# Performance work log

Hardware: AMD Instinct MI355X
Metric: run time of the kernel (lower is better)

The kernel has to match this reference:

```python
import jax, jax.numpy as jnp
import numpy as np

# WGS84 constants
_A = 6378137.0
_E2 = 6.69437999014e-3  # first eccentricity squared

ALPHA = 1.0
GAMMA = 2.0
DYNAMIC_GAMMA = True
SCALE_FACTOR = 1.0


def _geodetic_to_ecef(lat_rad, lon_rad, h):
    sl, cl = jnp.sin(lat_rad), jnp.cos(lat_rad)
    so, co = jnp.sin(lon_rad), jnp.cos(lon_rad)
    N = _A / jnp.sqrt(1.0 - _E2 * sl * sl)
    x = (N + h) * cl * co
    y = (N + h) * cl * so
    z = (N * (1.0 - _E2) + h) * sl
    return jnp.stack([x, y, z], axis=-1)


def setup_inputs() -> dict:
    key = jax.random.key(0)
    k1, k2, k3, k4 = jax.random.split(key, 4)
    B = 4_000_000
    lat = jax.random.uniform(k1, (B,), jnp.float32, -80.0, 80.0)    # degrees
    lon = jax.random.uniform(k2, (B,), jnp.float32, -180.0, 180.0)  # degrees
    h = jax.random.uniform(k3, (B,), jnp.float32, 0.0, 1000.0)      # meters
    targets = jnp.stack([lat, lon, h], axis=1)
    ref_ecef = _geodetic_to_ecef(jnp.deg2rad(lat), jnp.deg2rad(lon), h)
    # predicted ECEF = true ECEF + ~meters of noise -> realistic GNSS error
    inputs = ref_ecef + 2.0 * jax.random.normal(k4, (B, 3), jnp.float32)
    return {"inputs": inputs, "targets": targets}


def _ecef_to_enu(pred_ecef, gt_geodetic):
    # Batched version of the per-sample ecef_to_enu_torch loop.
    lat = jnp.deg2rad(gt_geodetic[:, 0])
    lon = jnp.deg2rad(gt_geodetic[:, 1])
    h = gt_geodetic[:, 2]
    ref = _geodetic_to_ecef(lat, lon, h)
    d = pred_ecef - ref  # [B,3]
    sl, cl = jnp.sin(lat), jnp.cos(lat)
    so, co = jnp.sin(lon), jnp.cos(lon)
    dx, dy, dz = d[:, 0], d[:, 1], d[:, 2]
    e = -so * dx + co * dy
    n = -sl * co * dx - sl * so * dy + cl * dz
    u = cl * co * dx + cl * so * dy + sl * dz
    return jnp.stack([e, n, u], axis=1)  # [B,3]


def reference(inputs, targets):
    enu_errors = _ecef_to_enu(inputs, targets)                 # [B,3]
    squared_dist = jnp.sqrt(jnp.sum(enu_errors * enu_errors, axis=1))  # L2 norm [B]
    base_loss = squared_dist
    if DYNAMIC_GAMMA:
        dyn_gamma = GAMMA * jnp.exp(-SCALE_FACTOR * base_loss)
    else:
        dyn_gamma = GAMMA
    focal_weight = jnp.power(1.0 - jnp.sqrt(squared_dist / (jnp.max(squared_dist) + 1e-8)), dyn_gamma)
    focal_loss = ALPHA * focal_weight * base_loss
    return jnp.sqrt(jnp.mean(focal_loss * focal_loss))
```

## Files before the change

### kernel.cpp

```cpp
#include <hip/hip_runtime.h>
#include <hip/hip_fp16.h>
#include <math.h>


#define THREADS 256
#define PART_CAP 8192
#define BMAX_OFF 64
#define PART_OFF (64 + PART_CAP * 4)
#define DIST_OFF (1 << 20)

__device__ __forceinline__ void sincos8(const double* __restrict__ x,
                                        double* __restrict__ s,
                                        double* __restrict__ c) {
    const double TWO_OVER_PI = 0.636619772367581343076;
    const double PIO2_HI = 1.57079632679489655800e+00;
    const double PIO2_LO = 6.12323399573676603587e-17;

    double kd[8], r[8], r2[8];
    int q[8];
#pragma unroll
    for (int j = 0; j < 8; ++j) {
        kd[j] = rint(x[j] * TWO_OVER_PI);
        q[j] = ((int)kd[j]) & 3;
    }
#pragma unroll
    for (int j = 0; j < 8; ++j) {
        double rr = fma(-kd[j], PIO2_HI, x[j]);
        r[j] = fma(-kd[j], PIO2_LO, rr);
        r2[j] = r[j] * r[j];
    }
    double ps[8], pc[8];
#pragma unroll
    for (int j = 0; j < 8; ++j) { ps[j] = -2.50507602534068634195e-08;
                                  pc[j] =  2.08757232129817482790e-09; }
#pragma unroll
    for (int j = 0; j < 8; ++j) { ps[j] = fma(ps[j], r2[j],  2.75573137070700676789e-06);
                                  pc[j] = fma(pc[j], r2[j], -2.75573143513906633035e-07); }
#pragma unroll
    for (int j = 0; j < 8; ++j) { ps[j] = fma(ps[j], r2[j], -1.98412698298579493134e-04);
                                  pc[j] = fma(pc[j], r2[j],  2.48015872894767294178e-05); }
#pragma unroll
    for (int j = 0; j < 8; ++j) { ps[j] = fma(ps[j], r2[j],  8.33333333332248946124e-03);
                                  pc[j] = fma(pc[j], r2[j], -1.38888888888741095749e-03); }
#pragma unroll
    for (int j = 0; j < 8; ++j) { ps[j] = fma(ps[j], r2[j], -1.66666666666666324348e-01);
                                  pc[j] = fma(pc[j], r2[j],  4.16666666666666019037e-02); }
#pragma unroll
    for (int j = 0; j < 8; ++j) {
        double sv = fma(r2[j] * r[j], ps[j], r[j]);
        double cv = fma(r2[j] * r2[j], pc[j], fma(-0.5, r2[j], 1.0));
        double sr = (q[j] & 1) ? cv : sv;
        double cr = (q[j] & 1) ? sv : cv;
        s[j] = (q[j] & 2) ? -sr : sr;
        c[j] = ((q[j] + 1) & 2) ? -cr : cr;
    }
}

__device__ __forceinline__ void dist_group4(const float* __restrict__ lat,
                                            const float* __restrict__ lon,
                                            const float* __restrict__ hh,
                                            const float* __restrict__ px,
                                            const float* __restrict__ py,
                                            const float* __restrict__ pz,
                                            float* __restrict__ dout) {
    const float D2R = (float)0.017453292519943295;
    double x[8], s8[8], c8[8];
#pragma unroll
    for (int j = 0; j < 4; ++j) x[j] = (double)(lat[j] * D2R);
#pragma unroll
    for (int j = 0; j < 4; ++j) x[4 + j] = (double)(lon[j] * D2R);
    sincos8(x, s8, c8);

    const double A = 6378137.0, E2 = 0.00669437999014;
#pragma unroll
    for (int j = 0; j < 4; ++j) {
        double sl = s8[j], cl = c8[j], so = s8[4 + j], co = c8[4 + j];
        double h = (double)hh[j];
        double w = fma(-E2 * sl, sl, 1.0);
        double y = fma(-0.5, w, 1.5);
        y = y * fma(-0.5 * w, y * y, 1.5);
        y = y * fma(-0.5 * w, y * y, 1.5);
        double N = A * y, Nh = N + h;
        double X = Nh * cl * co;
        double Y = Nh * cl * so;
        double Z = fma(N, -E2, N + h) * sl;
        double dx = (double)px[j] - X;
        double dy = (double)py[j] - Y;
        double dz = (double)pz[j] - Z;
        dout[j] = sqrtf((float)(dx * dx + dy * dy + dz * dz));
    }
}

__device__ __forceinline__ float dist_one(float latd, float lond, float hf,
                                          float pxx, float pyy, float pzz) {
    float lat[4] = {latd, latd, latd, latd}, lon[4] = {lond, lond, lond, lond};
    float hh[4] = {hf, hf, hf, hf};
    float px[4] = {pxx, pxx, pxx, pxx}, py[4] = {pyy, pyy, pyy, pyy}, pz[4] = {pzz, pzz, pzz, pzz};
    float d[4];
    dist_group4(lat, lon, hh, px, py, pz, d);
    return d[0];
}

#define UNPACK4(ta, tb, tc, lat, lon, hh)                         \
    float lat[4] = {ta.x, ta.w, tb.z, tc.y};                      \
    float lon[4] = {ta.y, tb.x, tb.w, tc.z};                      \
    float hh[4]  = {ta.z, tb.y, tc.x, tc.w};

__device__ __forceinline__ void store_half4(__half* p, float d0, float d1, float d2, float d3) {
    union { __half2 h2[2]; uint2 u; } pk;
    pk.h2[0] = __floats2half2_rn(d0, d1);
    pk.h2[1] = __floats2half2_rn(d2, d3);
    *(uint2*)p = pk.u;
}

__global__ __launch_bounds__(THREADS, 3)
void k_pass1(const float* __restrict__ inp, const float* __restrict__ tgt,
             __half* __restrict__ dist_arr, float* __restrict__ blockmax, long B) {
    long ngroups = (B + 3) >> 2;
    long nthreads = (long)gridDim.x * blockDim.x;
    long gstride = 2 * nthreads;
    float lmax = 0.0f;
    for (long g = (long)blockIdx.x * blockDim.x + threadIdx.x; g < ngroups; g += gstride) {
        long gA = g;
        long gB = g + nthreads;
        long baseA = gA << 2;
        long baseB = gB << 2;
        bool fastA = (baseA + 3 < B);
        bool fastB = (gB < ngroups) && (baseB + 3 < B);

        if (fastA && fastB) {
            const float4* tA = (const float4*)(tgt + 3 * baseA);
            const float4* pA = (const float4*)(inp + 3 * baseA);
            const float4* tB = (const float4*)(tgt + 3 * baseB);
            const float4* pB = (const float4*)(inp + 3 * baseB);
            float4 ta0 = tA[0], ta1 = tA[1], ta2 = tA[2];
            float4 pa0 = pA[0], pa1 = pA[1], pa2 = pA[2];
            float4 tb0 = tB[0], tb1 = tB[1], tb2 = tB[2];
            float4 pb0 = pB[0], pb1 = pB[1], pb2 = pB[2];

            UNPACK4(ta0, ta1, ta2, latA, lonA, hhA);
            UNPACK4(pa0, pa1, pa2, pxA, pyA, pzA);
            float dA[4];
            dist_group4(latA, lonA, hhA, pxA, pyA, pzA, dA);

            UNPACK4(tb0, tb1, tb2, latB, lonB, hhB);
            UNPACK4(pb0, pb1, pb2, pxB, pyB, pzB);
            float dB[4];
            dist_group4(latB, lonB, hhB, pxB, pyB, pzB, dB);

            if (dist_arr) {
                store_half4(dist_arr + baseA, dA[0], dA[1], dA[2], dA[3]);
                store_half4(dist_arr + baseB, dB[0], dB[1], dB[2], dB[3]);
            }
            lmax = fmaxf(lmax, fmaxf(fmaxf(dA[0], dA[1]), fmaxf(dA[2], dA[3])));
            lmax = fmaxf(lmax, fmaxf(fmaxf(dB[0], dB[1]), fmaxf(dB[2], dB[3])));
        } else {
            for (int pass = 0; pass < 2; ++pass) {
                long gg = pass ? gB : gA;
                if (gg >= ngroups) continue;
                long base = gg << 2;
                long end = base + 4 < B ? base + 4 : B;
                for (long i = base; i < end; ++i) {
                    float d = dist_one(tgt[3*i], tgt[3*i+1], tgt[3*i+2],
                                       inp[3*i], inp[3*i+1], inp[3*i+2]);
                    if (dist_arr) dist_arr[i] = __float2half_rn(d);
                    lmax = fmaxf(lmax, d);
                }
            }
        }
    }
    for (int off = 32; off > 0; off >>= 1)
        lmax = fmaxf(lmax, __shfl_down(lmax, off, 64));
    __shared__ float smax[THREADS / 64];
    if ((threadIdx.x & 63) == 0) smax[threadIdx.x >> 6] = lmax;
    __syncthreads();
    if (threadIdx.x == 0) {
        float m = smax[0];
        for (int w = 1; w < THREADS / 64; ++w) m = fmaxf(m, smax[w]);
        blockmax[blockIdx.x] = m;
    }
}

__device__ __forceinline__ double focal2(float d, float denom) {
    float g = 2.0f * __expf(-d);
    float b = 1.0f - sqrtf(d / denom);
    b = fmaxf(b, 0.0f);
    float wgt = __builtin_amdgcn_exp2f(g * __log2f(b));
    float fl = wgt * d;
    return (double)fl * (double)fl;
}

__global__ void k_pass2(const __half* __restrict__ dist_arr,
                        const float* __restrict__ inp,
                        const float* __restrict__ tgt,
                        const float* __restrict__ blockmax, int nb1,
                        double* __restrict__ partials, long B) {
    __shared__ float smax[THREADS / 64];
    __shared__ double sacc[THREADS / 64];
    __shared__ float sb;
    int tid = threadIdx.x;

    float m = 0.0f;
    for (int i = tid; i < nb1; i += THREADS) m = fmaxf(m, blockmax[i]);
    for (int off = 32; off > 0; off >>= 1)
        m = fmaxf(m, __shfl_down(m, off, 64));
    if ((tid & 63) == 0) smax[tid >> 6] = m;
    __syncthreads();
    if (tid == 0) {
        float mm = smax[0];
        for (int w = 1; w < THREADS / 64; ++w) mm = fmaxf(mm, smax[w]);
        sb = mm;
    }
    __syncthreads();
    float denom = sb + 1e-8f;

    long ngroups = (B + 3) >> 2;
    long gstride = (long)gridDim.x * blockDim.x;
    double acc = 0.0;
    for (long g = (long)blockIdx.x * blockDim.x + tid; g < ngroups; g += gstride) {
        long base = g << 2;
        if (base + 3 < B) {
            float d0, d1, d2, d3;
            if (dist_arr) {
                union { uint2 u; __half2 h2[2]; } pk;
                pk.u = *(const uint2*)(dist_arr + base);
                float2 lo = __half22float2(pk.h2[0]);
                float2 hi = __half22float2(pk.h2[1]);
                d0 = lo.x; d1 = lo.y; d2 = hi.x; d3 = hi.y;
            } else {
                const float4* t4 = (const float4*)(tgt + 3 * base);
                float4 ta = t4[0], tb = t4[1], tc = t4[2];
                const float4* p4 = (const float4*)(inp + 3 * base);
                float4 pa = p4[0], pb = p4[1], pc = p4[2];
                UNPACK4(ta, tb, tc, lat, lon, hh);
                UNPACK4(pa, pb, pc, px, py, pz);
                float d[4];
                dist_group4(lat, lon, hh, px, py, pz, d);
                d0 = d[0]; d1 = d[1]; d2 = d[2]; d3 = d[3];
            }
            acc += focal2(d0, denom) + focal2(d1, denom)
                 + focal2(d2, denom) + focal2(d3, denom);
        } else {
            for (long i = base; i < B; ++i) {
                float d = dist_arr ? __half2float(dist_arr[i])
                                   : dist_one(tgt[3*i], tgt[3*i+1], tgt[3*i+2],
                                              inp[3*i], inp[3*i+1], inp[3*i+2]);
                acc += focal2(d, denom);
            }
        }
    }
    for (int off = 32; off > 0; off >>= 1)
        acc += __shfl_down(acc, off, 64);
    if ((tid & 63) == 0) sacc[tid >> 6] = acc;
    __syncthreads();
    if (tid == 0) {
        double s = sacc[0];
        for (int w = 1; w < THREADS / 64; ++w) s += sacc[w];
        partials[blockIdx.x] = s;
    }
}

__global__ void k_final(const double* __restrict__ partials, int nparts,
                        float* __restrict__ out, long B) {
    double acc = 0.0;
    for (int i = threadIdx.x; i < nparts; i += blockDim.x) acc += partials[i];
    for (int off = 32; off > 0; off >>= 1)
        acc += __shfl_down(acc, off, 64);
    __shared__ double lds[THREADS / 64];
    if ((threadIdx.x & 63) == 0) lds[threadIdx.x >> 6] = acc;
    __syncthreads();
    if (threadIdx.x == 0) {
        double s = lds[0];
        for (int w = 1; w < THREADS / 64; ++w) s += lds[w];
        out[0] = (float)sqrt(s / (double)B);
    }
}

extern "C" void kernel_launch(void* const* d_in, const int* in_sizes, int n_in,
                              void* d_out, int out_size, void* d_ws, size_t ws_size,
                              hipStream_t stream) {
    const float* inp = (const float*)d_in[0];
    const float* tgt = (const float*)d_in[1];
    float* out = (float*)d_out;
    long B = (long)in_sizes[0] / 3;

    float* blockmax = (float*)((char*)d_ws + BMAX_OFF);
    double* partials = (double*)((char*)d_ws + PART_OFF);
    __half* dist_arr = nullptr;
    size_t need = (size_t)DIST_OFF + (size_t)B * sizeof(__half);
    if (ws_size >= need) dist_arr = (__half*)((char*)d_ws + DIST_OFF);

    long ngroups = (B + 3) >> 2;

    long nhalf = (ngroups + 1) >> 1;
    int nb1 = (int)((nhalf + THREADS - 1) / THREADS);
    if (nb1 > PART_CAP) nb1 = PART_CAP;
    if (nb1 < 1) nb1 = 1;

    int nb2 = (int)((ngroups + THREADS - 1) / THREADS);
    if (nb2 > PART_CAP) nb2 = PART_CAP;
    if (nb2 < 1) nb2 = 1;

    k_pass1<<<nb1, THREADS, 0, stream>>>(inp, tgt, dist_arr, blockmax, B);
    k_pass2<<<nb2, THREADS, 0, stream>>>(dist_arr, inp, tgt, blockmax, nb1, partials, B);
    k_final<<<1, THREADS, 0, stream>>>(partials, nb2, out, B);
}
```

Baseline: 130.5 us.

## Use float polynomial terms, float rsqrt seed, nontemporal loads, cap pass2 grid

```diff
diff --git a/kernel.cpp b/kernel.cpp
--- a/kernel.cpp
+++ b/kernel.cpp
@@ -5,9 +5,17 @@
 
 #define THREADS 256
 #define PART_CAP 8192
+#define NB2_CAP 2048
 #define BMAX_OFF 64
 #define PART_OFF (64 + PART_CAP * 4)
 #define DIST_OFF (1 << 20)
+
+typedef float f32x4 __attribute__((ext_vector_type(4)));
+
+__device__ __forceinline__ float4 ldnt4(const float* p) {
+    f32x4 v = __builtin_nontemporal_load((const f32x4*)p);
+    return make_float4(v.x, v.y, v.z, v.w);
+}
 
 __device__ __forceinline__ void sincos8(const double* __restrict__ x,
                                         double* __restrict__ s,
@@ -29,26 +37,27 @@
         r[j] = fma(-kd[j], PIO2_LO, rr);
         r2[j] = r[j] * r[j];
     }
-    double ps[8], pc[8];
-#pragma unroll
-    for (int j = 0; j < 8; ++j) { ps[j] = -2.50507602534068634195e-08;
-                                  pc[j] =  2.08757232129817482790e-09; }
-#pragma unroll
-    for (int j = 0; j < 8; ++j) { ps[j] = fma(ps[j], r2[j],  2.75573137070700676789e-06);
-                                  pc[j] = fma(pc[j], r2[j], -2.75573143513906633035e-07); }
-#pragma unroll
-    for (int j = 0; j < 8; ++j) { ps[j] = fma(ps[j], r2[j], -1.98412698298579493134e-04);
-                                  pc[j] = fma(pc[j], r2[j],  2.48015872894767294178e-05); }
-#pragma unroll
-    for (int j = 0; j < 8; ++j) { ps[j] = fma(ps[j], r2[j],  8.33333333332248946124e-03);
-                                  pc[j] = fma(pc[j], r2[j], -1.38888888888741095749e-03); }
-#pragma unroll
-    for (int j = 0; j < 8; ++j) { ps[j] = fma(ps[j], r2[j], -1.66666666666666324348e-01);
-                                  pc[j] = fma(pc[j], r2[j],  4.16666666666666019037e-02); }
+    float rf[8], psf[8], pcf[8];
+#pragma unroll
+    for (int j = 0; j < 8; ++j) rf[j] = (float)r2[j];
+#pragma unroll
+    for (int j = 0; j < 8; ++j) { psf[j] = -2.50507602534068634195e-08f;
+                                  pcf[j] =  2.08757232129817482790e-09f; }
+#pragma unroll
+    for (int j = 0; j < 8; ++j) { psf[j] = fmaf(psf[j], rf[j],  2.75573137070700676789e-06f);
+                                  pcf[j] = fmaf(pcf[j], rf[j], -2.75573143513906633035e-07f); }
+#pragma unroll
+    for (int j = 0; j < 8; ++j) { psf[j] = fmaf(psf[j], rf[j], -1.98412698298579493134e-04f);
+                                  pcf[j] = fmaf(pcf[j], rf[j],  2.48015872894767294178e-05f); }
+#pragma unroll
+    for (int j = 0; j < 8; ++j) { psf[j] = fmaf(psf[j], rf[j],  8.33333333332248946124e-03f);
+                                  pcf[j] = fmaf(pcf[j], rf[j], -1.38888888888741095749e-03f); }
 #pragma unroll
     for (int j = 0; j < 8; ++j) {
-        double sv = fma(r2[j] * r[j], ps[j], r[j]);
-        double cv = fma(r2[j] * r2[j], pc[j], fma(-0.5, r2[j], 1.0));
+        double ps = fma((double)psf[j], r2[j], -1.66666666666666324348e-01);
+        double pc = fma((double)pcf[j], r2[j],  4.16666666666666019037e-02);
+        double sv = fma(r2[j] * r[j], ps, r[j]);
+        double cv = fma(r2[j] * r2[j], pc, fma(-0.5, r2[j], 1.0));
         double sr = (q[j] & 1) ? cv : sv;
         double cr = (q[j] & 1) ? sv : cv;
         s[j] = (q[j] & 2) ? -sr : sr;
@@ -77,9 +86,8 @@
         double sl = s8[j], cl = c8[j], so = s8[4 + j], co = c8[4 + j];
         double h = (double)hh[j];
         double w = fma(-E2 * sl, sl, 1.0);
-        double y = fma(-0.5, w, 1.5);
-        y = y * fma(-0.5 * w, y * y, 1.5);
-        y = y * fma(-0.5 * w, y * y, 1.5);
+        double y0 = (double)__frsqrt_rn((float)w);
+        double y = y0 * fma(-0.5 * w, y0 * y0, 1.5);
         double N = A * y, Nh = N + h;
         double X = Nh * cl * co;
         double Y = Nh * cl * so;
@@ -129,14 +137,14 @@
         bool fastB = (gB < ngroups) && (baseB + 3 < B);
 
         if (fastA && fastB) {
-            const float4* tA = (const float4*)(tgt + 3 * baseA);
-            const float4* pA = (const float4*)(inp + 3 * baseA);
-            const float4* tB = (const float4*)(tgt + 3 * baseB);
-            const float4* pB = (const float4*)(inp + 3 * baseB);
-            float4 ta0 = tA[0], ta1 = tA[1], ta2 = tA[2];
-            float4 pa0 = pA[0], pa1 = pA[1], pa2 = pA[2];
-            float4 tb0 = tB[0], tb1 = tB[1], tb2 = tB[2];
-            float4 pb0 = pB[0], pb1 = pB[1], pb2 = pB[2];
+            const float* tA = tgt + 3 * baseA;
+            const float* pA = inp + 3 * baseA;
+            const float* tB = tgt + 3 * baseB;
+            const float* pB = inp + 3 * baseB;
+            float4 ta0 = ldnt4(tA), ta1 = ldnt4(tA + 4), ta2 = ldnt4(tA + 8);
+            float4 pa0 = ldnt4(pA), pa1 = ldnt4(pA + 4), pa2 = ldnt4(pA + 8);
+            float4 tb0 = ldnt4(tB), tb1 = ldnt4(tB + 4), tb2 = ldnt4(tB + 8);
+            float4 pb0 = ldnt4(pB), pb1 = ldnt4(pB + 4), pb2 = ldnt4(pB + 8);
 
             UNPACK4(ta0, ta1, ta2, latA, lonA, hhA);
             UNPACK4(pa0, pa1, pa2, pxA, pyA, pzA);
@@ -298,7 +306,7 @@
     if (nb1 < 1) nb1 = 1;
 
     int nb2 = (int)((ngroups + THREADS - 1) / THREADS);
-    if (nb2 > PART_CAP) nb2 = PART_CAP;
+    if (nb2 > NB2_CAP) nb2 = NB2_CAP;
     if (nb2 < 1) nb2 = 1;
 
     k_pass1<<<nb1, THREADS, 0, stream>>>(inp, tgt, dist_arr, blockmax, B);
```

New measurement: 138.4 us. 6.1% more time.
